# Kernel optimization log

Measured on AMD Instinct MI355X. Metric: run time of the kernel, lower is better.

The kernel has to match this reference:

```python
import jax, jax.numpy as jnp
import numpy as np

B, N, D, H = 4, 2048, 512, 8
DH = D // H
EPS = 1e-6


def setup_inputs() -> dict:
    key = jax.random.key(0)
    ks = jax.random.split(key, 12)
    s = 1.0 / np.sqrt(D)
    return {
        "x": jax.random.normal(ks[0], (B, N, D), jnp.float32),
        "attn_bias": jax.random.normal(ks[1], (B, 1, N, N), jnp.float32),
        "Wq": jax.random.normal(ks[2], (D, D), jnp.float32) * s,
        "bq": jnp.zeros((D,), jnp.float32),
        "Wk": jax.random.normal(ks[3], (D, D), jnp.float32) * s,
        "bk": jnp.zeros((D,), jnp.float32),
        "Wv": jax.random.normal(ks[4], (D, D), jnp.float32) * s,
        "bv": jnp.zeros((D,), jnp.float32),
        "Wo": jax.random.normal(ks[5], (D, D), jnp.float32) * s,
        "bo": jnp.zeros((D,), jnp.float32),
        "q_gamma": jnp.ones((DH,), jnp.float32),
        "q_beta": jnp.zeros((DH,), jnp.float32),
        "k_gamma": jnp.ones((DH,), jnp.float32),
        "k_beta": jnp.zeros((DH,), jnp.float32),
    }


def _layernorm(x, gamma, beta):
    mu = jnp.mean(x, axis=-1, keepdims=True)
    var = jnp.var(x, axis=-1, keepdims=True)
    return (x - mu) * jax.lax.rsqrt(var + EPS) * gamma + beta


def reference(x, attn_bias, Wq, bq, Wk, bk, Wv, bv, Wo, bo,
              q_gamma, q_beta, k_gamma, k_beta):
    b, n, d = x.shape
    # project and split heads: (B, H, N, DH)
    def heads(W, bias):
        return (x @ W.T + bias).reshape(b, n, H, DH).transpose(0, 2, 1, 3)
    q = heads(Wq, bq)
    k = heads(Wk, bk)
    v = heads(Wv, bv)
    q = _layernorm(q, q_gamma, q_beta)
    k = _layernorm(k, k_gamma, k_beta)
    scores = jnp.einsum('bhqd,bhkd->bhqk', q, k) / np.sqrt(DH)
    scores = scores + attn_bias  # (B,1,N,N) broadcasts over heads
    attn = jax.nn.softmax(scores, axis=-1)
    out = jnp.einsum('bhqk,bhkd->bhqd', attn, v)
    out = out.transpose(0, 2, 1, 3).reshape(b, n, d)
    return out @ Wo.T + bo
```

## Files before the change

kernel.cpp:

```cpp
#include <hip/hip_runtime.h>

typedef __attribute__((ext_vector_type(8))) short short8;
typedef __attribute__((ext_vector_type(4))) float f32x4;
typedef __attribute__((ext_vector_type(4))) int i32x4;
typedef __attribute__((ext_vector_type(4))) unsigned short u16x4;
typedef __attribute__((ext_vector_type(8))) unsigned short u16x8;
typedef __attribute__((ext_vector_type(2))) unsigned int u32x2;

#define B_  4
#define N_  2048
#define D_  512
#define H_  8
#define DH_ 64
#define M_  (B_ * N_)

__device__ __forceinline__ unsigned short f2bf(float f) {
    union { float f; unsigned u; } un; un.f = f;
    unsigned r = un.u + 0x7FFFu + ((un.u >> 16) & 1u);
    return (unsigned short)(r >> 16);
}
__device__ __forceinline__ unsigned packbf(float lo, float hi) {
    union { float f; unsigned u; } a, b;
    a.f = lo; b.f = hi;
    return __builtin_amdgcn_perm(b.u + 0x8000u, a.u + 0x8000u, 0x07060302u);
}
__device__ __forceinline__ float exp2fast(float x) {
#if __has_builtin(__builtin_amdgcn_exp2f)
    return __builtin_amdgcn_exp2f(x);
#else
    float r; asm("v_exp_f32 %0, %1" : "=v"(r) : "v"(x)); return r;
#endif
}

typedef __attribute__((address_space(1))) const void gvoid;
typedef __attribute__((address_space(3))) void svoid;
__device__ __forceinline__ void load16_lds(const void* g, void* s) {
    __builtin_amdgcn_global_load_lds((gvoid*)g, (svoid*)s, 16, 0, 0);
}

__global__ __launch_bounds__(256) void cvt_all(
    const float* __restrict__ x,
    const float* __restrict__ W0, const float* __restrict__ W1,
    const float* __restrict__ W2, const float* __restrict__ W3,
    unsigned short* __restrict__ xb, unsigned short* __restrict__ Wb) {
    const int bx = blockIdx.x;
    const float* src;
    unsigned short* dst;
    int i;
    if (bx < 4096) {
        src = x; dst = xb;
        i = (bx * 256 + (int)threadIdx.x) * 4;
    } else {
        const int r = bx - 4096;
        const int sel = r >> 8;
        src = (sel == 0) ? W0 : (sel == 1) ? W1 : (sel == 2) ? W2 : W3;
        dst = Wb + (size_t)sel * D_ * D_;
        i = ((r & 255) * 256 + (int)threadIdx.x) * 4;
    }
    f32x4 v = *(const f32x4*)(src + i);
    u16x4 o;
    o[0] = f2bf(v[0]); o[1] = f2bf(v[1]); o[2] = f2bf(v[2]); o[3] = f2bf(v[3]);
    *(u16x4*)(dst + i) = o;
}

template <bool F32OUT, bool LNF>
__global__ __launch_bounds__(256, 2) void gemm_nt(
    const unsigned short* __restrict__ A,
    const unsigned short* __restrict__ W,
    const float* __restrict__ Bv0,
    const float* __restrict__ Bv1,
    const float* __restrict__ Bv2,
    const float* __restrict__ g0, const float* __restrict__ be0,
    const float* __restrict__ g1, const float* __restrict__ be1,
    unsigned short* __restrict__ outb,
    float* __restrict__ outf)
{
    const int mt = blockIdx.x;
    const int nt = blockIdx.y;
    const int sel = nt >> 2;
    const unsigned short* Wp = W + (size_t)sel * D_ * D_;
    const float* Bv = (sel == 0) ? Bv0 : (sel == 1) ? Bv1 : Bv2;
    const int n0 = (nt & 3) * 128;

    __shared__ __align__(16) unsigned short As[128 * 32];
    __shared__ __align__(16) unsigned short Bs[128 * 32];

    const int tid = threadIdx.x;
    const int w   = tid >> 6;
    const int l   = tid & 63;
    const int l15 = l & 15;
    const int qd  = l >> 4;
    const int wr  = w >> 1;
    const int wc  = w & 1;

    int srow[2], scol[2];
#pragma unroll
    for (int c = 0; c < 2; ++c) {
        const int g   = (w * 2 + c) * 64 + l;
        const int row = g >> 2;
        srow[c] = row;
        scol[c] = ((g & 3) ^ (row & 3)) * 8;
    }

    f32x4 acc[4][4];
#pragma unroll
    for (int i = 0; i < 4; ++i)
#pragma unroll
        for (int j = 0; j < 4; ++j)
            acc[i][j] = (f32x4){0.f, 0.f, 0.f, 0.f};

    const int swz = qd ^ (l15 & 3);

    for (int k0 = 0; k0 < D_; k0 += 32) {
        __syncthreads();
#pragma unroll
        for (int c = 0; c < 2; ++c) {
            load16_lds(A  + (size_t)(mt * 128 + srow[c]) * D_ + k0 + scol[c],
                       As + (w * 2 + c) * 512);
            load16_lds(Wp + (size_t)(n0 + srow[c]) * D_ + k0 + scol[c],
                       Bs + (w * 2 + c) * 512);
        }
        __syncthreads();

        short8 af[4], bfr[4];
#pragma unroll
        for (int rt = 0; rt < 4; ++rt)
            af[rt] = *(const short8*)&As[(wr * 64 + rt * 16 + l15) * 32 + swz * 8];
#pragma unroll
        for (int ct = 0; ct < 4; ++ct)
            bfr[ct] = *(const short8*)&Bs[(wc * 64 + ct * 16 + l15) * 32 + swz * 8];
#pragma unroll
        for (int rt = 0; rt < 4; ++rt)
#pragma unroll
            for (int ct = 0; ct < 4; ++ct)
                acc[rt][ct] = __builtin_amdgcn_mfma_f32_16x16x32_bf16(
                    af[rt], bfr[ct], acc[rt][ct], 0, 0, 0);
    }

    const float* gam = (sel == 0) ? g0 : g1;
    const float* bet = (sel == 0) ? be0 : be1;
    float gv[4], bv2[4];
    if (LNF) {
#pragma unroll
        for (int ct = 0; ct < 4; ++ct) { gv[ct] = gam[ct * 16 + l15]; bv2[ct] = bet[ct * 16 + l15]; }
    }

#pragma unroll
    for (int rt = 0; rt < 4; ++rt) {
        float v[4][4];
#pragma unroll
        for (int ct = 0; ct < 4; ++ct) {
            const float bias = Bv[n0 + wc * 64 + ct * 16 + l15];
#pragma unroll
            for (int r = 0; r < 4; ++r) v[ct][r] = acc[rt][ct][r] + bias;
        }
        if (LNF && sel < 2) {
#pragma unroll
            for (int r = 0; r < 4; ++r) {
                float s  = v[0][r] + v[1][r] + v[2][r] + v[3][r];
                float s2 = v[0][r]*v[0][r] + v[1][r]*v[1][r] + v[2][r]*v[2][r] + v[3][r]*v[3][r];
#pragma unroll
                for (int o = 1; o <= 8; o <<= 1) {
                    s  += __shfl_xor(s, o);
                    s2 += __shfl_xor(s2, o);
                }
                const float mu  = s * 0.015625f;
                const float var = s2 * 0.015625f - mu * mu;
                const float rs  = rsqrtf(var + 1e-6f);
#pragma unroll
                for (int ct = 0; ct < 4; ++ct)
                    v[ct][r] = (v[ct][r] - mu) * rs * gv[ct] + bv2[ct];
            }
        }
#pragma unroll
        for (int ct = 0; ct < 4; ++ct) {
            const int col  = n0 + wc * 64 + ct * 16 + l15;
            const int row0 = mt * 128 + wr * 64 + rt * 16 + qd * 4;
#pragma unroll
            for (int r = 0; r < 4; ++r) {
                const size_t oidx = (size_t)(row0 + r) * D_ + col;
                if (F32OUT) outf[oidx] = v[ct][r];
                else        outb[(size_t)sel * M_ * D_ + oidx] = f2bf(v[ct][r]);
            }
        }
    }
}

__global__ __launch_bounds__(256) void pack_kv(
    const unsigned short* __restrict__ K, const unsigned short* __restrict__ V,
    unsigned short* __restrict__ Kt, unsigned short* __restrict__ Vt2)
{
    const int nt = blockIdx.x, b = blockIdx.y;
    const int tid = threadIdx.x;
    __shared__ __align__(16) unsigned short Vl[64][520];

#pragma unroll
    for (int i = 0; i < 16; ++i) {
        const int c = i * 256 + tid;
        const int row = c >> 6, ch = c & 63;
        const size_t srow = ((size_t)(b * N_ + nt * 64 + row)) * D_ + ch * 8;
        i32x4 kd = *(const i32x4*)(K + srow);
        const int h = ch >> 3, dc = ch & 7;
        *(i32x4*)(Kt + ((((size_t)(b * 8 + h) * 32 + nt) * 64 + row) * 64) + dc * 8) = kd;
        i32x4 vd = *(const i32x4*)(V + srow);
        *(i32x4*)&Vl[row][ch * 8] = vd;
    }
    __syncthreads();
#pragma unroll
    for (int i = 0; i < 16; ++i) {
        const int c = i * 256 + tid;
        const int h = c >> 9, r = c & 511;
        const int dh = r >> 3, kc = r & 7;
        u16x8 o;
#pragma unroll
        for (int j = 0; j < 8; ++j) o[j] = Vl[kc * 8 + j][h * 64 + dh];
        *(u16x8*)(Vt2 + ((((size_t)(b * 8 + h) * 32 + nt) * 64 + dh) * 64) + kc * 8) = o;
    }
}

__global__ __launch_bounds__(512, 4) void attn9(
    const unsigned short* __restrict__ Qm,
    const unsigned short* __restrict__ Kt,
    const unsigned short* __restrict__ Vt2,
    const float* __restrict__ Bias,
    unsigned short* __restrict__ AO)
{
    const int qt = blockIdx.x;
    const int h  = blockIdx.y;
    const int b  = blockIdx.z;
    const int w  = threadIdx.x >> 6;
    const int l  = threadIdx.x & 63;
    const int l15 = l & 15;
    const int qd  = l >> 4;
    const int q0 = qt * 128 + w * 16;

    __shared__ __align__(16) unsigned char smem[51200];
    unsigned short* PwB = (unsigned short*)(smem + 32768) + w * 16 * 72;

    const int c    = w * 64 + l;
    const int srow = c >> 3;
    const int sg   = (c & 7) ^ (srow & 7);
    const int soff = srow * 64 + sg * 8;
    const int sc16 = c * 16;

    short8 qf[2];
#pragma unroll
    for (int hf = 0; hf < 2; ++hf)
        qf[hf] = *(const short8*)(Qm +
            (size_t)(b * N_ + q0 + l15) * D_ + h * DH_ + hf * 32 + qd * 8);

    f32x4 Ot[4];
#pragma unroll
    for (int rt = 0; rt < 4; ++rt) Ot[rt] = (f32x4){0.f, 0.f, 0.f, 0.f};
    float m_i = -3.0e38f;
    float l_i = 0.f;

    const unsigned short* Ktile0 = Kt  + (((size_t)(b * 8 + h) * 32) * 64) * 64;
    const unsigned short* Vtile0 = Vt2 + (((size_t)(b * 8 + h) * 32) * 64) * 64;
    const float* biasQ = Bias + ((size_t)b * N_ + q0 + l15) * N_;

    load16_lds(Ktile0 + soff, smem + sc16);
    load16_lds(Vtile0 + soff, smem + 8192 + sc16);
    f32x4 brA[4], brB[4];
#pragma unroll
    for (int rt = 0; rt < 4; ++rt)
        brA[rt] = *(const f32x4*)(biasQ + rt * 16 + qd * 4);
    asm volatile("s_waitcnt vmcnt(0)" ::: "memory");

#define ATTN_ITER(KT, CUR, BRC, BRN) do {                                      \
    unsigned char* Kbc = smem + (CUR) * 16384;                                 \
    unsigned char* Vbc = Kbc + 8192;                                           \
    asm volatile("s_waitcnt vmcnt(4)" ::: "memory");                           \
    __builtin_amdgcn_s_barrier();                                              \
    __builtin_amdgcn_sched_barrier(0);                                         \
    if ((KT) < 31) {                                                           \
        const unsigned short* Kn = Ktile0 + (size_t)((KT) + 1) * 4096;         \
        const unsigned short* Vn = Vtile0 + (size_t)((KT) + 1) * 4096;         \
        unsigned char* KbN = smem + (((CUR) ^ 1)) * 16384;                     \
        load16_lds(Kn + soff, KbN + sc16);                                     \
        load16_lds(Vn + soff, KbN + 8192 + sc16);                              \
    }                                                                          \
    asm volatile("" ::: "memory");       \
    {                                                                          \
        const float* Bn = biasQ + (size_t)(((KT) < 31) ? (KT) + 1 : 31) * 64;  \
        _Pragma("unroll")                                                      \
        for (int rt = 0; rt < 4; ++rt)                                         \
            BRN[rt] = *(const f32x4*)(Bn + rt * 16 + qd * 4);                  \
    }                                                                          \
    short8 kf[4][2];                                                           \
    _Pragma("unroll")                                                          \
    for (int rt = 0; rt < 4; ++rt) {                                           \
        const int kv = rt * 16 + l15;                                          \
        _Pragma("unroll")                                                      \
        for (int hf = 0; hf < 2; ++hf) {                                       \
            const int cidx = (hf * 4 + qd) ^ (kv & 7);                         \
            kf[rt][hf] = *(const short8*)(Kbc + kv * 128 + cidx * 16);         \
        }                                                                      \
    }                                                                          \
    f32x4 St[4];                                                               \
    __builtin_amdgcn_s_setprio(1);                                             \
    _Pragma("unroll")                                                          \
    for (int rt = 0; rt < 4; ++rt) {                                           \
        f32x4 v = (f32x4){0.f, 0.f, 0.f, 0.f};                                 \
        v = __builtin_amdgcn_mfma_f32_16x16x32_bf16(kf[rt][0], qf[0], v, 0, 0, 0); \
        v = __builtin_amdgcn_mfma_f32_16x16x32_bf16(kf[rt][1], qf[1], v, 0, 0, 0); \
        St[rt] = v;                                                            \
    }                                                                          \
    __builtin_amdgcn_s_setprio(0);                                             \
    short8 vf[4][2];                                                           \
    _Pragma("unroll")                                                          \
    for (int rt = 0; rt < 4; ++rt) {                                           \
        const int dh = rt * 16 + l15;                                          \
        _Pragma("unroll")                                                      \
        for (int hf = 0; hf < 2; ++hf) {                                       \
            const int cidx = (hf * 4 + qd) ^ (dh & 7);                         \
            vf[rt][hf] = *(const short8*)(Vbc + dh * 128 + cidx * 16);         \
        }                                                                      \
    }                                                                          \
    {                                                                          \
        float sv[4][4];                                                        \
        float mx = -3.0e38f;                                                   \
        _Pragma("unroll")                                                      \
        for (int rt = 0; rt < 4; ++rt) {                                       \
            _Pragma("unroll")                                                  \
            for (int r = 0; r < 4; ++r) {                                      \
                sv[rt][r] = St[rt][r] * 0.1803368801f +                        \
                            BRC[rt][r] * 1.4426950408889634f;                  \
                mx = fmaxf(mx, sv[rt][r]);                                     \
            }                                                                  \
        }                                                                      \
        mx = fmaxf(mx, __shfl_xor(mx, 16));                                    \
        mx = fmaxf(mx, __shfl_xor(mx, 32));                                    \
        const float mnew  = fmaxf(m_i, mx);                                    \
        const float alpha = exp2fast(m_i - mnew);                              \
        float rsum = 0.f;                                                      \
        _Pragma("unroll")                                                      \
        for (int rt = 0; rt < 4; ++rt) {                                       \
            const float p0 = exp2fast(sv[rt][0] - mnew);                       \
            const float p1 = exp2fast(sv[rt][1] - mnew);                       \
            const float p2 = exp2fast(sv[rt][2] - mnew);                       \
            const float p3 = exp2fast(sv[rt][3] - mnew);                       \
            rsum += (p0 + p1) + (p2 + p3);                                     \
            u32x2 pw; pw[0] = packbf(p0, p1); pw[1] = packbf(p2, p3);          \
            *(u32x2*)&PwB[l15 * 72 + rt * 16 + qd * 4] = pw;                   \
        }                                                                      \
        l_i = l_i * alpha + rsum;                                              \
        m_i = mnew;                                                            \
        _Pragma("unroll")                                                      \
        for (int rt = 0; rt < 4; ++rt)                                         \
            _Pragma("unroll")                                                  \
            for (int r = 0; r < 4; ++r) Ot[rt][r] *= alpha;                    \
    }                                                                          \
    short8 pf[2];                                                              \
    _Pragma("unroll")                                                          \
    for (int hf = 0; hf < 2; ++hf)                                             \
        pf[hf] = *(const short8*)&PwB[l15 * 72 + hf * 32 + qd * 8];            \
    __builtin_amdgcn_s_setprio(1);                                             \
    _Pragma("unroll")                                                          \
    for (int rt = 0; rt < 4; ++rt) {                                           \
        Ot[rt] = __builtin_amdgcn_mfma_f32_16x16x32_bf16(vf[rt][0], pf[0], Ot[rt], 0, 0, 0); \
        Ot[rt] = __builtin_amdgcn_mfma_f32_16x16x32_bf16(vf[rt][1], pf[1], Ot[rt], 0, 0, 0); \
    }                                                                          \
    __builtin_amdgcn_s_setprio(0);                                             \
} while (0)

    for (int kt2 = 0; kt2 < 16; ++kt2) {
        ATTN_ITER(kt2 * 2,     0, brA, brB);
        ATTN_ITER(kt2 * 2 + 1, 1, brB, brA);
    }
#undef ATTN_ITER

    l_i += __shfl_xor(l_i, 16);
    l_i += __shfl_xor(l_i, 32);
    const float inv = 1.f / l_i;
    const int q = q0 + l15;
#pragma unroll
    for (int rt = 0; rt < 4; ++rt) {
        u16x4 ob;
#pragma unroll
        for (int r = 0; r < 4; ++r) ob[r] = f2bf(Ot[rt][r] * inv);
        *(u16x4*)(AO + (size_t)(b * N_ + q) * D_ + h * DH_ + rt * 16 + qd * 4) = ob;
    }
}

extern "C" void kernel_launch(void* const* d_in, const int* in_sizes, int n_in,
                              void* d_out, int out_size, void* d_ws, size_t ws_size,
                              hipStream_t stream) {
    const float* x  = (const float*)d_in[0];
    const float* ab = (const float*)d_in[1];
    const float* Wq = (const float*)d_in[2];
    const float* bq = (const float*)d_in[3];
    const float* Wk = (const float*)d_in[4];
    const float* bk = (const float*)d_in[5];
    const float* Wv = (const float*)d_in[6];
    const float* bv = (const float*)d_in[7];
    const float* Wo = (const float*)d_in[8];
    const float* bo = (const float*)d_in[9];
    const float* qg = (const float*)d_in[10];
    const float* qb = (const float*)d_in[11];
    const float* kg = (const float*)d_in[12];
    const float* kb = (const float*)d_in[13];

    unsigned short* xb  = (unsigned short*)d_ws;
    unsigned short* Wb  = xb  + (size_t)M_ * D_;
    unsigned short* Y   = Wb  + (size_t)4 * D_ * D_;
    unsigned short* Kt  = Y   + (size_t)3 * M_ * D_;
    unsigned short* Vt2 = Kt  + (size_t)M_ * D_;
    unsigned short* AO  = Vt2 + (size_t)M_ * D_;
    float* out = (float*)d_out;

    cvt_all<<<dim3(5120), dim3(256), 0, stream>>>(x, Wq, Wk, Wv, Wo, xb, Wb);

    gemm_nt<false, true><<<dim3(64, 12), dim3(256), 0, stream>>>(
        xb, Wb, bq, bk, bv, qg, qb, kg, kb, Y, nullptr);

    pack_kv<<<dim3(32, 4), dim3(256), 0, stream>>>(
        Y + (size_t)M_ * D_, Y + (size_t)2 * M_ * D_, Kt, Vt2);

    attn9<<<dim3(16, 8, 4), dim3(512), 0, stream>>>(
        Y, Kt, Vt2, ab, AO);

    gemm_nt<true, false><<<dim3(64, 4), dim3(256), 0, stream>>>(
        AO, Wb + (size_t)3 * D_ * D_, bo, bo, bo,
        nullptr, nullptr, nullptr, nullptr, nullptr, out);
}
```

Measured before the change: 254.8 us.

## Load K/V fragments directly to registers with software-pipelined PV across tiles

The attention kernel drops LDS staging of K/V tiles and block barriers. Each wave now loads K and V fragments straight from global memory into double-buffered registers, handles 32 query rows (two column tiles) per wave with 256-thread blocks, and defers the P·V MFMA by one iteration so the softmax of the current tile overlaps the previous tile's PV. The aim is to remove barrier stalls and LDS traffic and to reuse each K/V fragment across twice as many queries. In exchange, register pressure is much higher, which risks lower occupancy or spills, and every wave issues its own redundant global loads of K/V.

```diff
diff --git a/kernel.cpp b/kernel.cpp
--- a/kernel.cpp
+++ b/kernel.cpp
@@ -218,7 +218,7 @@
     }
 }
 
-__global__ __launch_bounds__(512, 4) void attn9(
+__global__ __launch_bounds__(256, 2) void attn10(
     const unsigned short* __restrict__ Qm,
     const unsigned short* __restrict__ Kt,
     const unsigned short* __restrict__ Vt2,
@@ -232,107 +232,121 @@
     const int l  = threadIdx.x & 63;
     const int l15 = l & 15;
     const int qd  = l >> 4;
-    const int q0 = qt * 128 + w * 16;
-
-    __shared__ __align__(16) unsigned char smem[51200];
-    unsigned short* PwB = (unsigned short*)(smem + 32768) + w * 16 * 72;
-
-    const int c    = w * 64 + l;
-    const int srow = c >> 3;
-    const int sg   = (c & 7) ^ (srow & 7);
-    const int soff = srow * 64 + sg * 8;
-    const int sc16 = c * 16;
-
-    short8 qf[2];
-#pragma unroll
-    for (int hf = 0; hf < 2; ++hf)
-        qf[hf] = *(const short8*)(Qm +
-            (size_t)(b * N_ + q0 + l15) * D_ + h * DH_ + hf * 32 + qd * 8);
-
-    f32x4 Ot[4];
-#pragma unroll
-    for (int rt = 0; rt < 4; ++rt) Ot[rt] = (f32x4){0.f, 0.f, 0.f, 0.f};
-    float m_i = -3.0e38f;
-    float l_i = 0.f;
+    const int q0 = qt * 128 + w * 32;
+
+    __shared__ __align__(16) unsigned short Pw[4 * 2 * 32 * 72];
+    unsigned short* Pw0 = Pw + (w * 2 + 0) * (32 * 72);
+    unsigned short* Pw1 = Pw + (w * 2 + 1) * (32 * 72);
+
+    short8 qf[2][2];
+#pragma unroll
+    for (int ct = 0; ct < 2; ++ct)
+#pragma unroll
+        for (int hf = 0; hf < 2; ++hf)
+            qf[ct][hf] = *(const short8*)(Qm +
+                (size_t)(b * N_ + q0 + ct * 16 + l15) * D_ + h * DH_ + hf * 32 + qd * 8);
+
+    f32x4 Ot[4][2];
+#pragma unroll
+    for (int rt = 0; rt < 4; ++rt)
+#pragma unroll
+        for (int ct = 0; ct < 2; ++ct) Ot[rt][ct] = (f32x4){0.f, 0.f, 0.f, 0.f};
+    float m_i[2] = {-3.0e38f, -3.0e38f};
+    float l_i[2] = {0.f, 0.f};
+    float al[2]  = {1.f, 1.f};
 
     const unsigned short* Ktile0 = Kt  + (((size_t)(b * 8 + h) * 32) * 64) * 64;
     const unsigned short* Vtile0 = Vt2 + (((size_t)(b * 8 + h) * 32) * 64) * 64;
-    const float* biasQ = Bias + ((size_t)b * N_ + q0 + l15) * N_;
-
-    load16_lds(Ktile0 + soff, smem + sc16);
-    load16_lds(Vtile0 + soff, smem + 8192 + sc16);
-    f32x4 brA[4], brB[4];
+    const int loff = l15 * 64 + qd * 8;
+    const float* bQ0 = Bias + ((size_t)b * N_ + q0 + l15) * N_;
+    const float* bQ1 = Bias + ((size_t)b * N_ + q0 + 16 + l15) * N_;
+
+    short8 kfA[4][2], kfB[4][2], vfA[4][2], vfB[4][2];
+
 #pragma unroll
     for (int rt = 0; rt < 4; ++rt)
-        brA[rt] = *(const f32x4*)(biasQ + rt * 16 + qd * 4);
-    asm volatile("s_waitcnt vmcnt(0)" ::: "memory");
-
-#define ATTN_ITER(KT, CUR, BRC, BRN) do {                                      \
-    unsigned char* Kbc = smem + (CUR) * 16384;                                 \
-    unsigned char* Vbc = Kbc + 8192;                                           \
-    asm volatile("s_waitcnt vmcnt(4)" ::: "memory");                           \
-    __builtin_amdgcn_s_barrier();                                              \
-    __builtin_amdgcn_sched_barrier(0);                                         \
-    if ((KT) < 31) {                                                           \
-        const unsigned short* Kn = Ktile0 + (size_t)((KT) + 1) * 4096;         \
-        const unsigned short* Vn = Vtile0 + (size_t)((KT) + 1) * 4096;         \
-        unsigned char* KbN = smem + (((CUR) ^ 1)) * 16384;                     \
-        load16_lds(Kn + soff, KbN + sc16);                                     \
-        load16_lds(Vn + soff, KbN + 8192 + sc16);                              \
-    }                                                                          \
-    asm volatile("" ::: "memory");       \
-    {                                                                          \
-        const float* Bn = biasQ + (size_t)(((KT) < 31) ? (KT) + 1 : 31) * 64;  \
-        _Pragma("unroll")                                                      \
-        for (int rt = 0; rt < 4; ++rt)                                         \
-            BRN[rt] = *(const f32x4*)(Bn + rt * 16 + qd * 4);                  \
-    }                                                                          \
-    short8 kf[4][2];                                                           \
+#pragma unroll
+        for (int hf = 0; hf < 2; ++hf)
+            kfA[rt][hf] = *(const short8*)(Ktile0 + rt * 1024 + loff + hf * 32);
+
+#define ATTN_ITER(T, KFC, KFN, VFC, VFP, PWC, PWP, DO_PV) do {                 \
+                      \
+    f32x4 br[4][2];                                                            \
     _Pragma("unroll")                                                          \
     for (int rt = 0; rt < 4; ++rt) {                                           \
-        const int kv = rt * 16 + l15;                                          \
-        _Pragma("unroll")                                                      \
-        for (int hf = 0; hf < 2; ++hf) {                                       \
-            const int cidx = (hf * 4 + qd) ^ (kv & 7);                         \
-            kf[rt][hf] = *(const short8*)(Kbc + kv * 128 + cidx * 16);         \
+        br[rt][0] = *(const f32x4*)(bQ0 + (T) * 64 + rt * 16 + qd * 4);        \
+        br[rt][1] = *(const f32x4*)(bQ1 + (T) * 64 + rt * 16 + qd * 4);        \
+    }                                                                          \
+                                                          \
+    {                                                                          \
+        const int ktn = ((T) < 31) ? (T) + 1 : 31;                             \
+        const unsigned short* Kn = Ktile0 + (size_t)ktn * 4096;                \
+        _Pragma("unroll")                                                      \
+        for (int rt = 0; rt < 4; ++rt)                                         \
+            _Pragma("unroll")                                                  \
+            for (int hf = 0; hf < 2; ++hf)                                     \
+                KFN[rt][hf] = *(const short8*)(Kn + rt * 1024 + loff + hf * 32); \
+    }                                                                          \
+                                    \
+    {                                                                          \
+        const unsigned short* Vn = Vtile0 + (size_t)(T) * 4096;                \
+        _Pragma("unroll")                                                      \
+        for (int rt = 0; rt < 4; ++rt)                                         \
+            _Pragma("unroll")                                                  \
+            for (int hf = 0; hf < 2; ++hf)                                     \
+                VFC[rt][hf] = *(const short8*)(Vn + rt * 1024 + loff + hf * 32); \
+    }                                                                          \
+                                                             \
+    f32x4 St[4][2];                                                            \
+    _Pragma("unroll")                                                          \
+    for (int rt = 0; rt < 4; ++rt)                                             \
+        _Pragma("unroll")                                                      \
+        for (int ct = 0; ct < 2; ++ct) {                                       \
+            f32x4 v = (f32x4){0.f, 0.f, 0.f, 0.f};                             \
+            v = __builtin_amdgcn_mfma_f32_16x16x32_bf16(KFC[rt][0], qf[ct][0], v, 0, 0, 0); \
+            v = __builtin_amdgcn_mfma_f32_16x16x32_bf16(KFC[rt][1], qf[ct][1], v, 0, 0, 0); \
+            St[rt][ct] = v;                                                    \
         }                                                                      \
+    if (DO_PV) {                                                               \
+                       \
+        _Pragma("unroll")                                                      \
+        for (int rt = 0; rt < 4; ++rt)                                         \
+            _Pragma("unroll")                                                  \
+            for (int ct = 0; ct < 2; ++ct)                                     \
+                _Pragma("unroll")                                              \
+                for (int r = 0; r < 4; ++r) Ot[rt][ct][r] *= al[ct];           \
+        short8 pf[2][2];                                                       \
+        _Pragma("unroll")                                                      \
+        for (int ct = 0; ct < 2; ++ct)                                         \
+            _Pragma("unroll")                                                  \
+            for (int hf = 0; hf < 2; ++hf)                                     \
+                pf[ct][hf] = *(const short8*)&PWP[(ct * 16 + l15) * 72 + hf * 32 + qd * 8]; \
+        _Pragma("unroll")                                                      \
+        for (int rt = 0; rt < 4; ++rt)                                         \
+            _Pragma("unroll")                                                  \
+            for (int ct = 0; ct < 2; ++ct) {                                   \
+                Ot[rt][ct] = __builtin_amdgcn_mfma_f32_16x16x32_bf16(VFP[rt][0], pf[ct][0], Ot[rt][ct], 0, 0, 0); \
+                Ot[rt][ct] = __builtin_amdgcn_mfma_f32_16x16x32_bf16(VFP[rt][1], pf[ct][1], Ot[rt][ct], 0, 0, 0); \
+            }                                                                  \
     }                                                                          \
-    f32x4 St[4];                                                               \
-    __builtin_amdgcn_s_setprio(1);                                             \
+      \
     _Pragma("unroll")                                                          \
-    for (int rt = 0; rt < 4; ++rt) {                                           \
-        f32x4 v = (f32x4){0.f, 0.f, 0.f, 0.f};                                 \
-        v = __builtin_amdgcn_mfma_f32_16x16x32_bf16(kf[rt][0], qf[0], v, 0, 0, 0); \
-        v = __builtin_amdgcn_mfma_f32_16x16x32_bf16(kf[rt][1], qf[1], v, 0, 0, 0); \
-        St[rt] = v;                                                            \
-    }                                                                          \
-    __builtin_amdgcn_s_setprio(0);                                             \
-    short8 vf[4][2];                                                           \
-    _Pragma("unroll")                                                          \
-    for (int rt = 0; rt < 4; ++rt) {                                           \
-        const int dh = rt * 16 + l15;                                          \
-        _Pragma("unroll")                                                      \
-        for (int hf = 0; hf < 2; ++hf) {                                       \
-            const int cidx = (hf * 4 + qd) ^ (dh & 7);                         \
-            vf[rt][hf] = *(const short8*)(Vbc + dh * 128 + cidx * 16);         \
-        }                                                                      \
-    }                                                                          \
-    {                                                                          \
+    for (int ct = 0; ct < 2; ++ct) {                                           \
         float sv[4][4];                                                        \
         float mx = -3.0e38f;                                                   \
         _Pragma("unroll")                                                      \
         for (int rt = 0; rt < 4; ++rt) {                                       \
             _Pragma("unroll")                                                  \
             for (int r = 0; r < 4; ++r) {                                      \
-                sv[rt][r] = St[rt][r] * 0.1803368801f +                        \
-                            BRC[rt][r] * 1.4426950408889634f;                  \
+                sv[rt][r] = St[rt][ct][r] * 0.1803368801f +                    \
+                            br[rt][ct][r] * 1.4426950408889634f;               \
                 mx = fmaxf(mx, sv[rt][r]);                                     \
             }                                                                  \
         }                                                                      \
         mx = fmaxf(mx, __shfl_xor(mx, 16));                                    \
         mx = fmaxf(mx, __shfl_xor(mx, 32));                                    \
-        const float mnew  = fmaxf(m_i, mx);                                    \
-        const float alpha = exp2fast(m_i - mnew);                              \
+        const float mnew = fmaxf(m_i[ct], mx);                                 \
+        al[ct] = exp2fast(m_i[ct] - mnew);                                     \
         float rsum = 0.f;                                                      \
         _Pragma("unroll")                                                      \
         for (int rt = 0; rt < 4; ++rt) {                                       \
@@ -342,44 +356,57 @@
             const float p3 = exp2fast(sv[rt][3] - mnew);                       \
             rsum += (p0 + p1) + (p2 + p3);                                     \
             u32x2 pw; pw[0] = packbf(p0, p1); pw[1] = packbf(p2, p3);          \
-            *(u32x2*)&PwB[l15 * 72 + rt * 16 + qd * 4] = pw;                   \
+            *(u32x2*)&PWC[(ct * 16 + l15) * 72 + rt * 16 + qd * 4] = pw;       \
         }                                                                      \
-        l_i = l_i * alpha + rsum;                                              \
-        m_i = mnew;                                                            \
-        _Pragma("unroll")                                                      \
-        for (int rt = 0; rt < 4; ++rt)                                         \
-            _Pragma("unroll")                                                  \
-            for (int r = 0; r < 4; ++r) Ot[rt][r] *= alpha;                    \
+        l_i[ct] = l_i[ct] * al[ct] + rsum;                                     \
+        m_i[ct] = mnew;                                                        \
     }                                                                          \
-    short8 pf[2];                                                              \
-    _Pragma("unroll")                                                          \
-    for (int hf = 0; hf < 2; ++hf)                                             \
-        pf[hf] = *(const short8*)&PwB[l15 * 72 + hf * 32 + qd * 8];            \
-    __builtin_amdgcn_s_setprio(1);                                             \
-    _Pragma("unroll")                                                          \
-    for (int rt = 0; rt < 4; ++rt) {                                           \
-        Ot[rt] = __builtin_amdgcn_mfma_f32_16x16x32_bf16(vf[rt][0], pf[0], Ot[rt], 0, 0, 0); \
-        Ot[rt] = __builtin_amdgcn_mfma_f32_16x16x32_bf16(vf[rt][1], pf[1], Ot[rt], 0, 0, 0); \
-    }                                                                          \
-    __builtin_amdgcn_s_setprio(0);                                             \
 } while (0)
 
-    for (int kt2 = 0; kt2 < 16; ++kt2) {
-        ATTN_ITER(kt2 * 2,     0, brA, brB);
-        ATTN_ITER(kt2 * 2 + 1, 1, brB, brA);
-    }
+    ATTN_ITER(0, kfA, kfB, vfA, vfB, Pw0, Pw1, false);
+    for (int kt2 = 0; kt2 < 15; ++kt2) {
+        const int t1 = kt2 * 2 + 1;
+        ATTN_ITER(t1,     kfB, kfA, vfB, vfA, Pw1, Pw0, true);
+        ATTN_ITER(t1 + 1, kfA, kfB, vfA, vfB, Pw0, Pw1, true);
+    }
+    ATTN_ITER(31, kfB, kfA, vfB, vfA, Pw1, Pw0, true);
 #undef ATTN_ITER
 
-    l_i += __shfl_xor(l_i, 16);
-    l_i += __shfl_xor(l_i, 32);
-    const float inv = 1.f / l_i;
-    const int q = q0 + l15;
-#pragma unroll
-    for (int rt = 0; rt < 4; ++rt) {
-        u16x4 ob;
-#pragma unroll
-        for (int r = 0; r < 4; ++r) ob[r] = f2bf(Ot[rt][r] * inv);
-        *(u16x4*)(AO + (size_t)(b * N_ + q) * D_ + h * DH_ + rt * 16 + qd * 4) = ob;
+    {
+#pragma unroll
+        for (int rt = 0; rt < 4; ++rt)
+#pragma unroll
+            for (int ct = 0; ct < 2; ++ct)
+#pragma unroll
+                for (int r = 0; r < 4; ++r) Ot[rt][ct][r] *= al[ct];
+        short8 pf[2][2];
+#pragma unroll
+        for (int ct = 0; ct < 2; ++ct)
+#pragma unroll
+            for (int hf = 0; hf < 2; ++hf)
+                pf[ct][hf] = *(const short8*)&Pw1[(ct * 16 + l15) * 72 + hf * 32 + qd * 8];
+#pragma unroll
+        for (int rt = 0; rt < 4; ++rt)
+#pragma unroll
+            for (int ct = 0; ct < 2; ++ct) {
+                Ot[rt][ct] = __builtin_amdgcn_mfma_f32_16x16x32_bf16(vfB[rt][0], pf[ct][0], Ot[rt][ct], 0, 0, 0);
+                Ot[rt][ct] = __builtin_amdgcn_mfma_f32_16x16x32_bf16(vfB[rt][1], pf[ct][1], Ot[rt][ct], 0, 0, 0);
+            }
+    }
+
+#pragma unroll
+    for (int ct = 0; ct < 2; ++ct) {
+        l_i[ct] += __shfl_xor(l_i[ct], 16);
+        l_i[ct] += __shfl_xor(l_i[ct], 32);
+        const float inv = 1.f / l_i[ct];
+        const int q = q0 + ct * 16 + l15;
+#pragma unroll
+        for (int rt = 0; rt < 4; ++rt) {
+            u16x4 ob;
+#pragma unroll
+            for (int r = 0; r < 4; ++r) ob[r] = f2bf(Ot[rt][ct][r] * inv);
+            *(u16x4*)(AO + (size_t)(b * N_ + q) * D_ + h * DH_ + rt * 16 + qd * 4) = ob;
+        }
     }
 }
 
@@ -417,7 +444,7 @@
     pack_kv<<<dim3(32, 4), dim3(256), 0, stream>>>(
         Y + (size_t)M_ * D_, Y + (size_t)2 * M_ * D_, Kt, Vt2);
 
-    attn9<<<dim3(16, 8, 4), dim3(512), 0, stream>>>(
+    attn10<<<dim3(16, 8, 4), dim3(256), 0, stream>>>(
         Y, Kt, Vt2, ab, AO);
 
     gemm_nt<true, false><<<dim3(64, 4), dim3(256), 0, stream>>>(
```

Result: slower. 346.9 us (+36.2%).

## Use lazy softmax rescaling, hardware bf16 pack, max3 reduction in attention

Applied to the files above, without the earlier changes.

Rewrites the online-softmax step in the attention kernel. The running max and the O/l rescale are updated only when some lane's new max exceeds the old one by more than a threshold (a wave-wide branch), so the alpha exp and the Ot scaling are skipped on most iterations. Row sums accumulate as a 4-wide vector and are reduced once at the end. The manual perm-based bf16 packing is replaced with v_cvt_pk_bf16_f32, and the max reduction uses three-input max patterns. The cost is an extra multiply per element to apply log2(e) after subtracting the max, plus an accepted bounded growth of unnormalized probabilities that could affect bf16 precision.

```diff
diff --git a/kernel.cpp b/kernel.cpp
--- a/kernel.cpp
+++ b/kernel.cpp
@@ -19,17 +19,20 @@
     unsigned r = un.u + 0x7FFFu + ((un.u >> 16) & 1u);
     return (unsigned short)(r >> 16);
 }
-__device__ __forceinline__ unsigned packbf(float lo, float hi) {
-    union { float f; unsigned u; } a, b;
-    a.f = lo; b.f = hi;
-    return __builtin_amdgcn_perm(b.u + 0x8000u, a.u + 0x8000u, 0x07060302u);
-}
 __device__ __forceinline__ float exp2fast(float x) {
 #if __has_builtin(__builtin_amdgcn_exp2f)
     return __builtin_amdgcn_exp2f(x);
 #else
     float r; asm("v_exp_f32 %0, %1" : "=v"(r) : "v"(x)); return r;
 #endif
+}
+__device__ __forceinline__ unsigned cvtpk_bf16(float lo, float hi) {
+    unsigned r;
+    asm("v_cvt_pk_bf16_f32 %0, %1, %2" : "=v"(r) : "v"(lo), "v"(hi));
+    return r;
+}
+__device__ __forceinline__ float max3f(float a, float b, float c) {
+    return fmaxf(fmaxf(a, b), c);
 }
 
 typedef __attribute__((address_space(1))) const void gvoid;
@@ -218,7 +221,7 @@
     }
 }
 
-__global__ __launch_bounds__(512, 4) void attn9(
+__global__ __launch_bounds__(512, 4) void attn11(
     const unsigned short* __restrict__ Qm,
     const unsigned short* __restrict__ Kt,
     const unsigned short* __restrict__ Vt2,
@@ -233,6 +236,7 @@
     const int l15 = l & 15;
     const int qd  = l >> 4;
     const int q0 = qt * 128 + w * 16;
+    const float L2E = 1.4426950408889634f;
 
     __shared__ __align__(16) unsigned char smem[51200];
     unsigned short* PwB = (unsigned short*)(smem + 32768) + w * 16 * 72;
@@ -253,7 +257,7 @@
 #pragma unroll
     for (int rt = 0; rt < 4; ++rt) Ot[rt] = (f32x4){0.f, 0.f, 0.f, 0.f};
     float m_i = -3.0e38f;
-    float l_i = 0.f;
+    f32x4 li4 = (f32x4){0.f, 0.f, 0.f, 0.f};
 
     const unsigned short* Ktile0 = Kt  + (((size_t)(b * 8 + h) * 32) * 64) * 64;
     const unsigned short* Vtile0 = Vt2 + (((size_t)(b * 8 + h) * 32) * 64) * 64;
@@ -318,38 +322,46 @@
         }                                                                      \
     }                                                                          \
     {                                                                          \
-        float sv[4][4];                                                        \
-        float mx = -3.0e38f;                                                   \
-        _Pragma("unroll")                                                      \
-        for (int rt = 0; rt < 4; ++rt) {                                       \
-            _Pragma("unroll")                                                  \
-            for (int r = 0; r < 4; ++r) {                                      \
-                sv[rt][r] = St[rt][r] * 0.1803368801f +                        \
-                            BRC[rt][r] * 1.4426950408889634f;                  \
-                mx = fmaxf(mx, sv[rt][r]);                                     \
-            }                                                                  \
-        }                                                                      \
+                      \
+        f32x4 sv[4];                                                           \
+        _Pragma("unroll")                                                      \
+        for (int rt = 0; rt < 4; ++rt)                                         \
+            sv[rt] = St[rt] * 0.125f + BRC[rt];                                \
+                                                  \
+        float mx0 = max3f(sv[0][0], sv[0][1], sv[0][2]);                       \
+        float mx1 = max3f(sv[0][3], sv[1][0], sv[1][1]);                       \
+        float mx2 = max3f(sv[1][2], sv[1][3], sv[2][0]);                       \
+        float mx3 = max3f(sv[2][1], sv[2][2], sv[2][3]);                       \
+        mx0 = max3f(mx0, sv[3][0], sv[3][1]);                                  \
+        mx1 = max3f(mx1, sv[3][2], sv[3][3]);                                  \
+        float mx = fmaxf(max3f(mx0, mx1, mx2), mx3);                           \
         mx = fmaxf(mx, __shfl_xor(mx, 16));                                    \
         mx = fmaxf(mx, __shfl_xor(mx, 32));                                    \
-        const float mnew  = fmaxf(m_i, mx);                                    \
-        const float alpha = exp2fast(m_i - mnew);                              \
-        float rsum = 0.f;                                                      \
+                \
+        if (__any(mx > m_i + 8.0f)) {                                          \
+            const float mnew  = fmaxf(m_i, mx);                                \
+            const float alpha = exp2fast((m_i - mnew) * L2E);                  \
+            m_i = mnew;                                                        \
+            li4 *= alpha;                                                      \
+            _Pragma("unroll")                                                  \
+            for (int rt = 0; rt < 4; ++rt) Ot[rt] *= alpha;                    \
+        }                                                                      \
+        const float mL = m_i * L2E;                                            \
+        f32x4 p[4];                                                            \
         _Pragma("unroll")                                                      \
         for (int rt = 0; rt < 4; ++rt) {                                       \
-            const float p0 = exp2fast(sv[rt][0] - mnew);                       \
-            const float p1 = exp2fast(sv[rt][1] - mnew);                       \
-            const float p2 = exp2fast(sv[rt][2] - mnew);                       \
-            const float p3 = exp2fast(sv[rt][3] - mnew);                       \
-            rsum += (p0 + p1) + (p2 + p3);                                     \
-            u32x2 pw; pw[0] = packbf(p0, p1); pw[1] = packbf(p2, p3);          \
+            f32x4 e = sv[rt] * L2E - mL;                           \
+            p[rt][0] = exp2fast(e[0]); p[rt][1] = exp2fast(e[1]);              \
+            p[rt][2] = exp2fast(e[2]); p[rt][3] = exp2fast(e[3]);              \
+        }                                                                      \
+        li4 += (p[0] + p[1]) + (p[2] + p[3]);                                  \
+        _Pragma("unroll")                                                      \
+        for (int rt = 0; rt < 4; ++rt) {                                       \
+            u32x2 pw;                                                          \
+            pw[0] = cvtpk_bf16(p[rt][0], p[rt][1]);                            \
+            pw[1] = cvtpk_bf16(p[rt][2], p[rt][3]);                            \
             *(u32x2*)&PwB[l15 * 72 + rt * 16 + qd * 4] = pw;                   \
         }                                                                      \
-        l_i = l_i * alpha + rsum;                                              \
-        m_i = mnew;                                                            \
-        _Pragma("unroll")                                                      \
-        for (int rt = 0; rt < 4; ++rt)                                         \
-            _Pragma("unroll")                                                  \
-            for (int r = 0; r < 4; ++r) Ot[rt][r] *= alpha;                    \
     }                                                                          \
     short8 pf[2];                                                              \
     _Pragma("unroll")                                                          \
@@ -370,6 +382,7 @@
     }
 #undef ATTN_ITER
 
+    float l_i = (li4[0] + li4[1]) + (li4[2] + li4[3]);
     l_i += __shfl_xor(l_i, 16);
     l_i += __shfl_xor(l_i, 32);
     const float inv = 1.f / l_i;
@@ -417,7 +430,7 @@
     pack_kv<<<dim3(32, 4), dim3(256), 0, stream>>>(
         Y + (size_t)M_ * D_, Y + (size_t)2 * M_ * D_, Kt, Vt2);
 
-    attn9<<<dim3(16, 8, 4), dim3(512), 0, stream>>>(
+    attn11<<<dim3(16, 8, 4), dim3(512), 0, stream>>>(
         Y, Kt, Vt2, ab, AO);
 
     gemm_nt<true, false><<<dim3(64, 4), dim3(256), 0, stream>>>(
```

New measurement: 257.1 us. About the same (+0.9%).
